# Performance work log

Measured on AMD Instinct MI355X. Metric: run time of the kernel, lower is better.

Reference implementation:

```python
import jax, jax.numpy as jnp
import numpy as np

D_MODEL = 1024
N_HEADS = 16
HEAD_DIM = 64  # 16*64 = 1024
LATENT = 256   # low-rank KV compression dim
NUM_WHEELS = 4
WHEEL_OUT = 256


def setup_inputs() -> dict:
    key = jax.random.key(0)
    ks = jax.random.split(key, 9)
    S = 2048
    s = lambda fan_in: 1.0 / np.sqrt(fan_in)
    return {
        "sketch_emb": jax.random.normal(ks[0], (S, D_MODEL), dtype=jnp.float32),
        "Wq": jax.random.normal(ks[1], (D_MODEL, N_HEADS * HEAD_DIM), dtype=jnp.float32) * s(D_MODEL),
        "Wdkv": jax.random.normal(ks[2], (D_MODEL, LATENT), dtype=jnp.float32) * s(D_MODEL),
        "Wuk": jax.random.normal(ks[3], (LATENT, N_HEADS * HEAD_DIM), dtype=jnp.float32) * s(LATENT),
        "Wuv": jax.random.normal(ks[4], (LATENT, N_HEADS * HEAD_DIM), dtype=jnp.float32) * s(LATENT),
        "Wo": jax.random.normal(ks[5], (N_HEADS * HEAD_DIM, D_MODEL), dtype=jnp.float32) * s(N_HEADS * HEAD_DIM),
        "wheel_W": jax.random.normal(ks[6], (NUM_WHEELS, D_MODEL, WHEEL_OUT), dtype=jnp.float32) * s(D_MODEL),
        "wheel_b": jax.random.normal(ks[7], (NUM_WHEELS, WHEEL_OUT), dtype=jnp.float32) * 0.01,
    }


def reference(sketch_emb, Wq, Wdkv, Wuk, Wuv, Wo, wheel_W, wheel_b):
    S = sketch_emb.shape[0]
    # Multi-head latent attention: per-head Q, shared low-rank KV latent.
    q = (sketch_emb @ Wq).reshape(S, N_HEADS, HEAD_DIM)          # [S,H,D]
    c_kv = sketch_emb @ Wdkv                                      # [S,L]
    k = (c_kv @ Wuk).reshape(S, N_HEADS, HEAD_DIM)                # [S,H,D]
    v = (c_kv @ Wuv).reshape(S, N_HEADS, HEAD_DIM)                # [S,H,D]
    scale = 1.0 / np.sqrt(HEAD_DIM).astype(np.float32)
    scores = jnp.einsum("qhd,khd->hqk", q, k) * scale             # [H,S,S]
    attn = jax.nn.softmax(scores, axis=-1)
    ctx = jnp.einsum("hqk,khd->qhd", attn, v).reshape(S, N_HEADS * HEAD_DIM)
    body = ctx @ Wo                                               # [S,1024]
    # Wheel projections batched as one einsum, then laid out as concat order
    # cat([body, w0, w1, w2, w3], dim=1)
    wheels = jnp.einsum("sd,wde->swe", body, wheel_W) + wheel_b   # [S,W,256]
    wheels = wheels.reshape(S, NUM_WHEELS * WHEEL_OUT)
    return jnp.concatenate([body, wheels], axis=1)                # [S,2048]
```

## Files before the change

### kernel.cpp

```cpp
#include <hip/hip_runtime.h>
#include <math.h>

#define S_LEN 2048
#define DMODEL 1024
#define NHEADS 16
#define HDIM 64
#define QPITCH 1280

typedef _Float16 f16x8 __attribute__((ext_vector_type(8)));
typedef _Float16 f16x4 __attribute__((ext_vector_type(4)));
typedef float    f32x4 __attribute__((ext_vector_type(4)));

__device__ __forceinline__ void gld_lds16(void* lds, const void* g) {
    __builtin_amdgcn_global_load_lds(
        (__attribute__((address_space(1))) void*)(g),
        (__attribute__((address_space(3))) void*)(lds), 16, 0, 0);
}

__device__ __forceinline__ void gemm_core(
    _Float16* sA, _Float16* sB,
    const _Float16* __restrict__ A, int lda,
    const _Float16* __restrict__ Bt, int ldb,
    int nkt,
    _Float16* __restrict__ Cb, int ldcb, int bmode,
    _Float16* __restrict__ Cb2, int ldcb2,
    int bx, int by)
{
    const int tid  = threadIdx.x;
    const int lane = tid & 63;
    const int w    = tid >> 6;
    const int quad = lane >> 4;
    const int c0   = lane & 15;
    const int m0 = by * 128;
    const int n0 = bx * 128;

    const int srow = lane >> 3;
    const int sc   = lane & 7;
    const _Float16* a_src[4]; const _Float16* b_src[4];
    int dstoff[4];
#pragma unroll
    for (int t = 0; t < 4; t++) {
        const int row = w * 32 + t * 8 + srow;
        const int c = sc ^ (row & 7);
        a_src[t] = A  + (size_t)(m0 + row) * lda + c * 8;
        b_src[t] = Bt + (size_t)(n0 + row) * ldb + c * 8;
        dstoff[t] = (w * 32 + t * 8) * 64;
    }

    const int mw = (w & 1) * 64;
    const int nw = (w >> 1) * 64;
    int arow[4], brow[4];
#pragma unroll
    for (int i = 0; i < 4; i++) {
        arow[i] = mw + i * 16 + c0;
        brow[i] = nw + i * 16 + c0;
    }

    f32x4 acc[4][4];
#pragma unroll
    for (int i = 0; i < 4; i++)
#pragma unroll
        for (int j = 0; j < 4; j++) acc[i][j] = (f32x4){0.f, 0.f, 0.f, 0.f};

    auto stage = [&](int buf) {
#pragma unroll
        for (int t = 0; t < 4; t++) {
            gld_lds16(&sA[buf * 8192 + dstoff[t]], a_src[t]); a_src[t] += 64;
            gld_lds16(&sB[buf * 8192 + dstoff[t]], b_src[t]); b_src[t] += 64;
        }
    };
    auto step = [&](int buf) {
#pragma unroll
        for (int ks = 0; ks < 2; ks++) {
            const int cb = ks * 4 + quad;
            f16x8 af[4], bfv[4];
#pragma unroll
            for (int i = 0; i < 4; i++)
                af[i] = *(const f16x8*)&sA[buf * 8192 + arow[i] * 64 + ((cb ^ (arow[i] & 7)) << 3)];
#pragma unroll
            for (int j = 0; j < 4; j++)
                bfv[j] = *(const f16x8*)&sB[buf * 8192 + brow[j] * 64 + ((cb ^ (brow[j] & 7)) << 3)];
#pragma unroll
            for (int i = 0; i < 4; i++)
#pragma unroll
                for (int j = 0; j < 4; j++)
                    acc[i][j] = __builtin_amdgcn_mfma_f32_16x16x32_f16(af[i], bfv[j], acc[i][j], 0, 0, 0);
        }
    };

    stage(0);
    for (int kt = 0; kt < nkt; kt += 2) {
        __syncthreads();
        stage(1);
        step(0);
        __syncthreads();
        if (kt + 2 < nkt) stage(0);
        step(1);
    }

#pragma unroll
    for (int i = 0; i < 4; i++) {
#pragma unroll
        for (int reg = 0; reg < 4; reg++) {
            const int m = m0 + mw + i * 16 + quad * 4 + reg;
#pragma unroll
            for (int j = 0; j < 4; j++) {
                const int n = n0 + nw + j * 16 + c0;
                _Float16 hv = (_Float16)acc[i][j][reg];
                if (bmode == 0) {
                    Cb[(size_t)m * ldcb + n] = hv;
                } else {
                    if (n < 1024) Cb[(size_t)m * ldcb + n] = hv;
                    else {
                        const int col = (m & ~63) | (((m & 15) << 2) | ((m >> 4) & 3));
                        Cb2[(size_t)(n - 1024) * ldcb2 + col] = hv;
                    }
                }
            }
        }
    }
}

__global__ __launch_bounds__(256) void gemm_qcwf(
    const _Float16* __restrict__ WcT, const _Float16* __restrict__ Wo_f16,
    _Float16* __restrict__ BtWheels,
    const _Float16* __restrict__ emb_f16, const _Float16* __restrict__ Wqc_t,
    _Float16* __restrict__ qc_f16)
{
    __shared__ _Float16 sA[2][8192];
    __shared__ _Float16 sB[2][8192];
    int b = blockIdx.x;
    if (b < 64) {
        gemm_core(&sA[0][0], &sB[0][0], WcT, 1024, Wo_f16, 1024, 16,
                  BtWheels, 1024, 0, nullptr, 0, b & 7, b >> 3);
    } else {
        b -= 64;
        gemm_core(&sA[0][0], &sB[0][0], emb_f16, 1024, Wqc_t, 1024, 16,
                  qc_f16, 1280, 0, nullptr, 0, b % 10, b / 10);
    }
}

__global__ __launch_bounds__(256) void gemm_kv(
    const _Float16* __restrict__ qc_f16, const _Float16* __restrict__ Wukv_t,
    _Float16* __restrict__ k_f16, _Float16* __restrict__ vT_f16)
{
    __shared__ _Float16 sA[2][8192];
    __shared__ _Float16 sB[2][8192];
    const int b = blockIdx.x;
    gemm_core(&sA[0][0], &sB[0][0], qc_f16 + 1024, 1280, Wukv_t, 256, 4,
              k_f16, 1024, 4, vT_f16, 2048, b & 15, b >> 4);
}

__global__ __launch_bounds__(256) void gemm_fin64(
    const _Float16* __restrict__ A,
    const _Float16* __restrict__ Bt,
    float* __restrict__ out,
    const float* __restrict__ bias)
{
    __shared__ _Float16 sA[2][64 * 64];
    __shared__ _Float16 sB[2][128 * 64];

    const int tid  = threadIdx.x;
    const int lane = tid & 63;
    const int w    = tid >> 6;
    const int quad = lane >> 4;
    const int c0   = lane & 15;
    const int m0 = blockIdx.y * 64;
    const int n0 = blockIdx.x * 128;

    const int srow = lane >> 3;
    const int sc   = lane & 7;
    const _Float16* a_src[2]; int a_dst[2];
#pragma unroll
    for (int t = 0; t < 2; t++) {
        const int row = t * 32 + w * 8 + srow;
        const int c = sc ^ (row & 7);
        a_src[t] = A + (size_t)(m0 + row) * 1024 + c * 8;
        a_dst[t] = (t * 32 + w * 8) * 64;
    }
    const _Float16* b_src[4]; int b_dst[4];
#pragma unroll
    for (int t = 0; t < 4; t++) {
        const int row = t * 32 + w * 8 + srow;
        const int c = sc ^ (row & 7);
        b_src[t] = Bt + (size_t)(n0 + row) * 1024 + c * 8;
        b_dst[t] = (t * 32 + w * 8) * 64;
    }

    const int mw = (w & 1) * 32;
    const int nw = (w >> 1) * 64;
    int arow[2], brow[4];
#pragma unroll
    for (int i = 0; i < 2; i++) arow[i] = mw + i * 16 + c0;
#pragma unroll
    for (int j = 0; j < 4; j++) brow[j] = nw + j * 16 + c0;

    f32x4 acc[2][4];
#pragma unroll
    for (int i = 0; i < 2; i++)
#pragma unroll
        for (int j = 0; j < 4; j++) acc[i][j] = (f32x4){0.f, 0.f, 0.f, 0.f};

    auto stage = [&](int buf) {
#pragma unroll
        for (int t = 0; t < 2; t++) { gld_lds16(&sA[buf][a_dst[t]], a_src[t]); a_src[t] += 64; }
#pragma unroll
        for (int t = 0; t < 4; t++) { gld_lds16(&sB[buf][b_dst[t]], b_src[t]); b_src[t] += 64; }
    };
    auto step = [&](int buf) {
#pragma unroll
        for (int ks = 0; ks < 2; ks++) {
            const int cb = ks * 4 + quad;
            f16x8 af[2], bfv[4];
#pragma unroll
            for (int i = 0; i < 2; i++)
                af[i] = *(const f16x8*)&sA[buf][arow[i] * 64 + ((cb ^ (arow[i] & 7)) << 3)];
#pragma unroll
            for (int j = 0; j < 4; j++)
                bfv[j] = *(const f16x8*)&sB[buf][brow[j] * 64 + ((cb ^ (brow[j] & 7)) << 3)];
#pragma unroll
            for (int i = 0; i < 2; i++)
#pragma unroll
                for (int j = 0; j < 4; j++)
                    acc[i][j] = __builtin_amdgcn_mfma_f32_16x16x32_f16(af[i], bfv[j], acc[i][j], 0, 0, 0);
        }
    };

    stage(0);
    for (int kt = 0; kt < 16; kt += 2) {
        __syncthreads();
        stage(1);
        step(0);
        __syncthreads();
        if (kt + 2 < 16) stage(0);
        step(1);
    }

    float bias_v[4];
#pragma unroll
    for (int j = 0; j < 4; j++) bias_v[j] = bias[n0 + nw + j * 16 + c0];
#pragma unroll
    for (int i = 0; i < 2; i++) {
#pragma unroll
        for (int reg = 0; reg < 4; reg++) {
            const int m = m0 + mw + i * 16 + quad * 4 + reg;
#pragma unroll
            for (int j = 0; j < 4; j++) {
                const int n = n0 + nw + j * 16 + c0;
                out[(size_t)m * 2048 + n] = acc[i][j][reg] + bias_v[j];
            }
        }
    }
}

#define PITCH 72
#define SOFT_M0 6.0f

__global__ __launch_bounds__(256) void attn_mfma_kernel(
    const _Float16* __restrict__ qs,
    const _Float16* __restrict__ kk,
    const _Float16* __restrict__ vT,
    float* __restrict__ Opart,
    float* __restrict__ lpart)
{
    __shared__ _Float16 Ks[2][64 * 64];
    __shared__ _Float16 Vt[2][64 * 64];
    __shared__ _Float16 Ps[4 * 32 * PITCH];

    const int qb = blockIdx.x;
    const int h  = blockIdx.y;
    const int kz = blockIdx.z;
    const int tid  = threadIdx.x;
    const int lane = tid & 63;
    const int w    = tid >> 6;
    const int quad = lane >> 4;
    const int c0   = lane & 15;

    f16x8 qfrag[2][2];
#pragma unroll
    for (int m = 0; m < 2; m++) {
        const _Float16* qrow = qs + (size_t)(qb * 128 + w * 32 + m * 16 + c0) * QPITCH + h * HDIM;
        qfrag[m][0] = *(const f16x8*)(qrow + quad * 8);
        qfrag[m][1] = *(const f16x8*)(qrow + 32 + quad * 8);
    }

    const int srow = lane >> 3;
    const int sc   = lane & 7;
    const _Float16* k_src[2]; const _Float16* v_src[2];
    int dstoff[2];
#pragma unroll
    for (int t = 0; t < 2; t++) {
        const int row = w * 16 + t * 8 + srow;
        const int c = sc ^ (row & 7);
        k_src[t] = kk + (size_t)(kz * 1024 + row) * DMODEL + h * HDIM + c * 8;
        v_src[t] = vT + (size_t)(h * HDIM + row) * S_LEN + kz * 1024 + c * 8;
        dstoff[t] = (w * 16 + t * 8) * 64;
    }

    f32x4 Ofrag[2][4];
#pragma unroll
    for (int m = 0; m < 2; m++)
#pragma unroll
        for (int nb = 0; nb < 4; nb++) Ofrag[m][nb] = (f32x4){0.f, 0.f, 0.f, 0.f};
    float l_r[2][4] = {{0.f, 0.f, 0.f, 0.f}, {0.f, 0.f, 0.f, 0.f}};

    _Float16* Pw = Ps + w * (32 * PITCH);

    auto stage = [&](int buf) {
#pragma unroll
        for (int t = 0; t < 2; t++) {
            gld_lds16(&Ks[buf][dstoff[t]], k_src[t]); k_src[t] += (size_t)64 * DMODEL;
            gld_lds16(&Vt[buf][dstoff[t]], v_src[t]); v_src[t] += 64;
        }
    };

    auto attn_step = [&](int buf) {
        f32x4 sfrag[2][4];
#pragma unroll
        for (int m = 0; m < 2; m++)
#pragma unroll
            for (int nb = 0; nb < 4; nb++) sfrag[m][nb] = (f32x4){0.f, 0.f, 0.f, 0.f};
#pragma unroll
        for (int nb = 0; nb < 4; nb++) {
            const int n = nb * 16 + c0;
#pragma unroll
            for (int ks = 0; ks < 2; ks++) {
                const int cb = ks * 4 + quad;
                f16x8 kfr = *(const f16x8*)&Ks[buf][n * 64 + ((cb ^ (n & 7)) << 3)];
#pragma unroll
                for (int m = 0; m < 2; m++)
                    sfrag[m][nb] = __builtin_amdgcn_mfma_f32_16x16x32_f16(qfrag[m][ks], kfr, sfrag[m][nb], 0, 0, 0);
            }
        }

#pragma unroll
        for (int m = 0; m < 2; m++)
#pragma unroll
            for (int reg = 0; reg < 4; reg++) {
                float p0 = __expf(sfrag[m][0][reg] - SOFT_M0);
                float p1 = __expf(sfrag[m][1][reg] - SOFT_M0);
                float p2 = __expf(sfrag[m][2][reg] - SOFT_M0);
                float p3 = __expf(sfrag[m][3][reg] - SOFT_M0);
                sfrag[m][0][reg] = p0; sfrag[m][1][reg] = p1;
                sfrag[m][2][reg] = p2; sfrag[m][3][reg] = p3;
                l_r[m][reg] += p0 + p1 + p2 + p3;
            }

#pragma unroll
        for (int m = 0; m < 2; m++)
#pragma unroll
            for (int reg = 0; reg < 4; reg++) {
                const int prow = m * 16 + quad * 4 + reg;
                f16x4 pv;
                pv[0] = (_Float16)sfrag[m][0][reg];
                pv[1] = (_Float16)sfrag[m][1][reg];
                pv[2] = (_Float16)sfrag[m][2][reg];
                pv[3] = (_Float16)sfrag[m][3][reg];
                *(f16x4*)&Pw[prow * PITCH + c0 * 4] = pv;
            }
        __asm__ __volatile__("s_waitcnt lgkmcnt(0)" ::: "memory");

        f16x8 pfrag[2][2];
#pragma unroll
        for (int m = 0; m < 2; m++)
#pragma unroll
            for (int ks = 0; ks < 2; ks++)
                pfrag[m][ks] = *(const f16x8*)&Pw[(m * 16 + c0) * PITCH + ks * 32 + quad * 8];

#pragma unroll
        for (int nb = 0; nb < 4; nb++) {
            const int n = nb * 16 + c0;
#pragma unroll
            for (int ks = 0; ks < 2; ks++) {
                const int cb = ks * 4 + quad;
                f16x8 vf = *(const f16x8*)&Vt[buf][n * 64 + ((cb ^ (n & 7)) << 3)];
#pragma unroll
                for (int m = 0; m < 2; m++)
                    Ofrag[m][nb] = __builtin_amdgcn_mfma_f32_16x16x32_f16(pfrag[m][ks], vf, Ofrag[m][nb], 0, 0, 0);
            }
        }
    };

    stage(0);
    for (int kt = 0; kt < 16; kt += 2) {
        __syncthreads();
        stage(1);
        attn_step(0);
        __syncthreads();
        if (kt + 2 < 16) stage(0);
        attn_step(1);
    }

#pragma unroll
    for (int m = 0; m < 2; m++) {
#pragma unroll
        for (int reg = 0; reg < 4; reg++) {
            const int row = qb * 128 + w * 32 + m * 16 + quad * 4 + reg;
            float rsum = l_r[m][reg];
#pragma unroll
            for (int mask = 1; mask < 16; mask <<= 1)
                rsum += __shfl_xor(rsum, mask, 64);
            if (c0 == 0) lpart[(size_t)(kz * 16 + h) * 2048 + row] = rsum;
            float* op = Opart + ((size_t)kz * 2048 + row) * 1024 + h * HDIM;
#pragma unroll
            for (int nb = 0; nb < 4; nb++)
                op[nb * 16 + c0] = Ofrag[m][nb][reg];
        }
    }
}

__global__ __launch_bounds__(256) void attn_combine_kernel(
    const float* __restrict__ Opart, const float* __restrict__ lpart,
    _Float16* __restrict__ ctx)
{
    const int i = blockIdx.x * 256 + threadIdx.x;
    const int row = i >> 8;
    const int c4  = (i & 255) * 4;
    const int h = c4 >> 6;
    const float l = lpart[(size_t)h * 2048 + row] + lpart[(size_t)(16 + h) * 2048 + row];
    const float inv = 1.0f / l;
    float4 o0 = ((const float4*)(Opart + (size_t)row * 1024))[c4 >> 2];
    float4 o1 = ((const float4*)(Opart + (size_t)(2048 + row) * 1024))[c4 >> 2];
    f16x4 v;
    v[0] = (_Float16)((o0.x + o1.x) * inv);
    v[1] = (_Float16)((o0.y + o1.y) * inv);
    v[2] = (_Float16)((o0.z + o1.z) * inv);
    v[3] = (_Float16)((o0.w + o1.w) * inv);
    *(f16x4*)(ctx + (size_t)row * 1024 + c4) = v;
}

__device__ __forceinline__ void xpose_seg(float (*tile)[33],
    const float* __restrict__ src, _Float16* __restrict__ dst,
    int C, int dpitch, float scale, int bx, int by, int nbase0)
{
    const int r0 = by * 32, c0 = bx * 32;
    const int tr = threadIdx.x >> 5, tc = threadIdx.x & 31;
#pragma unroll
    for (int i = 0; i < 4; i++)
        tile[tr + i * 8][tc] = src[(size_t)(r0 + tr + i * 8) * C + c0 + tc];
    __syncthreads();
    const int nr = threadIdx.x & 31;
    const int k0 = (threadIdx.x >> 5) * 4;
    f16x4 hv;
#pragma unroll
    for (int e = 0; e < 4; e++)
        hv[e] = (_Float16)(tile[k0 + e][nr] * scale);
    *(f16x4*)(dst + (size_t)(nbase0 + c0 + nr) * dpitch + (r0 + k0)) = hv;
}

__global__ __launch_bounds__(256) void megaprep_kernel(
    const float* __restrict__ emb, const float* __restrict__ Wq,
    const float* __restrict__ Wdkv, const float* __restrict__ Wuk,
    const float* __restrict__ Wuv, const float* __restrict__ Wo,
    const float* __restrict__ wheelW, const float* __restrict__ wheelB,
    _Float16* __restrict__ Wqc_t, _Float16* __restrict__ Wukv_t,
    _Float16* __restrict__ Bt_full, _Float16* __restrict__ WcT,
    _Float16* __restrict__ Wo_f16, _Float16* __restrict__ emb_f16,
    float* __restrict__ biasbuf)
{
    __shared__ float tile[32][33];
    int b = blockIdx.x;
    const int tid = threadIdx.x;

    if (b < 1024) { xpose_seg(tile, Wq, Wqc_t, 1024, 1024, 0.125f, b & 31, b >> 5, 0); return; }
    b -= 1024;
    if (b < 256)  { xpose_seg(tile, Wdkv, Wqc_t + 1048576, 256, 1024, 1.f, b & 7, b >> 3, 0); return; }
    b -= 256;
    if (b < 256)  { xpose_seg(tile, Wuk, Wukv_t, 1024, 256, 1.f, b & 31, b >> 5, 0); return; }
    b -= 256;
    if (b < 256)  { xpose_seg(tile, Wuv, Wukv_t + 262144, 1024, 256, 1.f, b & 31, b >> 5, 0); return; }
    b -= 256;
    if (b < 1024) { xpose_seg(tile, Wo, Bt_full, 1024, 1024, 1.f, b & 31, b >> 5, 0); return; }
    b -= 1024;
    if (b < 1024) {
        const int z = b >> 8, rem = b & 255;
        xpose_seg(tile, wheelW + (size_t)z * 262144, WcT, 256, 1024, 1.f,
                  rem & 7, rem >> 3, z * 256);
        return;
    }
    b -= 1024;
    if (b < 1024) {
        const int i = b * 256 + tid;
        float4 f = ((const float4*)Wo)[i];
        f16x4 v;
        v[0] = (_Float16)f.x; v[1] = (_Float16)f.y;
        v[2] = (_Float16)f.z; v[3] = (_Float16)f.w;
        ((f16x4*)Wo_f16)[i] = v;
        return;
    }
    b -= 1024;
    if (b < 2048) {
        const int i = b * 256 + tid;
        float4 f = ((const float4*)emb)[i];
        f16x4 v;
        v[0] = (_Float16)f.x; v[1] = (_Float16)f.y;
        v[2] = (_Float16)f.z; v[3] = (_Float16)f.w;
        ((f16x4*)emb_f16)[i] = v;
        return;
    }
    b -= 2048;
    if (b < 8) {
        const int i = b * 256 + tid;
        biasbuf[i] = (i < 1024) ? 0.f : wheelB[i - 1024];
    }
}

extern "C" void kernel_launch(void* const* d_in, const int* in_sizes, int n_in,
                              void* d_out, int out_size, void* d_ws, size_t ws_size,
                              hipStream_t stream) {
    const float* emb    = (const float*)d_in[0];
    const float* Wq     = (const float*)d_in[1];
    const float* Wdkv   = (const float*)d_in[2];
    const float* Wuk    = (const float*)d_in[3];
    const float* Wuv    = (const float*)d_in[4];
    const float* Wo     = (const float*)d_in[5];
    const float* wheelW = (const float*)d_in[6];
    const float* wheelB = (const float*)d_in[7];
    float* out = (float*)d_out;

    _Float16* ws = (_Float16*)d_ws;
    _Float16* Bt_full = ws;
    _Float16* Wqc_t   = ws + 2097152;
    _Float16* Wukv_t  = ws + 3407872;
    float*    biasbuf = (float*)(ws + 3932160);
    _Float16* WcT     = ws + 3936256;
    _Float16* Wo_f16  = ws + 4984832;
    _Float16* ctx     = ws + 3936256;
    _Float16* emb_f16 = ws + 6033408;
    _Float16* qc_f16  = ws + 8130560;
    _Float16* k_f16   = ws + 10752000;
    _Float16* vT_f16  = ws + 12849152;
    float*    Opart   = (float*)(ws + 14946304);
    float*    lpart   = (float*)(ws + 23334912);

    megaprep_kernel<<<6920, 256, 0, stream>>>(
        emb, Wq, Wdkv, Wuk, Wuv, Wo, wheelW, wheelB,
        Wqc_t, Wukv_t, Bt_full, WcT, Wo_f16, emb_f16, biasbuf);

    gemm_qcwf<<<224, 256, 0, stream>>>(WcT, Wo_f16, Bt_full + (size_t)1024 * 1024,
                                       emb_f16, Wqc_t, qc_f16);

    gemm_kv<<<256, 256, 0, stream>>>(qc_f16, Wukv_t, k_f16, vT_f16);

    attn_mfma_kernel<<<dim3(16, 16, 2), 256, 0, stream>>>(qc_f16, k_f16, vT_f16, Opart, lpart);

    attn_combine_kernel<<<2048, 256, 0, stream>>>(Opart, lpart, ctx);

    gemm_fin64<<<dim3(16, 32), 256, 0, stream>>>(ctx, Bt_full, out, biasbuf);
}
```

Before: 175.0 us.

## Remap block indices for XCD locality, use exp2 softmax, add MFMA priority hints

Block-to-tile mappings in the GEMM kernels and the attention kernel are remapped: grids are flattened and swizzled so blocks sharing operands land on the same XCD, aiming for better L2 reuse. The softmax switches from __expf to the native exp2 instruction, with log2(e) folded into the Wuk weights during prep and a matching constant offset. s_setprio hints are placed around the MFMA loops. The changes are independent, and the new index mappings rely on fixed grid sizes.

```diff
diff --git a/kernel.cpp b/kernel.cpp
--- a/kernel.cpp
+++ b/kernel.cpp
@@ -132,11 +132,11 @@
     int b = blockIdx.x;
     if (b < 64) {
         gemm_core(&sA[0][0], &sB[0][0], WcT, 1024, Wo_f16, 1024, 16,
-                  BtWheels, 1024, 0, nullptr, 0, b & 7, b >> 3);
+                  BtWheels, 1024, 0, nullptr, 0, b >> 3, b & 7);
     } else {
         b -= 64;
         gemm_core(&sA[0][0], &sB[0][0], emb_f16, 1024, Wqc_t, 1024, 16,
-                  qc_f16, 1280, 0, nullptr, 0, b % 10, b / 10);
+                  qc_f16, 1280, 0, nullptr, 0, b >> 4, b & 15);
     }
 }
 
@@ -148,7 +148,7 @@
     __shared__ _Float16 sB[2][8192];
     const int b = blockIdx.x;
     gemm_core(&sA[0][0], &sB[0][0], qc_f16 + 1024, 1280, Wukv_t, 256, 4,
-              k_f16, 1024, 4, vT_f16, 2048, b & 15, b >> 4);
+              k_f16, 1024, 4, vT_f16, 2048, b >> 4, b & 15);
 }
 
 __global__ __launch_bounds__(256) void gemm_fin64(
@@ -165,8 +165,14 @@
     const int w    = tid >> 6;
     const int quad = lane >> 4;
     const int c0   = lane & 15;
-    const int m0 = blockIdx.y * 64;
-    const int n0 = blockIdx.x * 128;
+
+    const int flat = blockIdx.x;
+    const int xcd  = flat & 7;
+    const int wi   = flat >> 3;
+    const int by   = (xcd & 3) * 8 + (wi & 7);
+    const int bx   = (xcd >> 2) * 8 + (wi >> 3);
+    const int m0 = by * 64;
+    const int n0 = bx * 128;
 
     const int srow = lane >> 3;
     const int sc   = lane & 7;
@@ -254,7 +260,7 @@
 }
 
 #define PITCH 72
-#define SOFT_M0 6.0f
+#define SOFT_M2 8.65617024533378f
 
 __global__ __launch_bounds__(256) void attn_mfma_kernel(
     const _Float16* __restrict__ qs,
@@ -267,9 +273,11 @@
     __shared__ _Float16 Vt[2][64 * 64];
     __shared__ _Float16 Ps[4 * 32 * PITCH];
 
-    const int qb = blockIdx.x;
-    const int h  = blockIdx.y;
-    const int kz = blockIdx.z;
+    const int flat = blockIdx.x;
+    const int g  = flat & 31;
+    const int qb = flat >> 5;
+    const int h  = g & 15;
+    const int kz = g >> 4;
     const int tid  = threadIdx.x;
     const int lane = tid & 63;
     const int w    = tid >> 6;
@@ -320,6 +328,7 @@
         for (int m = 0; m < 2; m++)
 #pragma unroll
             for (int nb = 0; nb < 4; nb++) sfrag[m][nb] = (f32x4){0.f, 0.f, 0.f, 0.f};
+        __builtin_amdgcn_s_setprio(1);
 #pragma unroll
         for (int nb = 0; nb < 4; nb++) {
             const int n = nb * 16 + c0;
@@ -332,15 +341,16 @@
                     sfrag[m][nb] = __builtin_amdgcn_mfma_f32_16x16x32_f16(qfrag[m][ks], kfr, sfrag[m][nb], 0, 0, 0);
             }
         }
+        __builtin_amdgcn_s_setprio(0);
 
 #pragma unroll
         for (int m = 0; m < 2; m++)
 #pragma unroll
             for (int reg = 0; reg < 4; reg++) {
-                float p0 = __expf(sfrag[m][0][reg] - SOFT_M0);
-                float p1 = __expf(sfrag[m][1][reg] - SOFT_M0);
-                float p2 = __expf(sfrag[m][2][reg] - SOFT_M0);
-                float p3 = __expf(sfrag[m][3][reg] - SOFT_M0);
+                float p0 = __builtin_amdgcn_exp2f(sfrag[m][0][reg] - SOFT_M2);
+                float p1 = __builtin_amdgcn_exp2f(sfrag[m][1][reg] - SOFT_M2);
+                float p2 = __builtin_amdgcn_exp2f(sfrag[m][2][reg] - SOFT_M2);
+                float p3 = __builtin_amdgcn_exp2f(sfrag[m][3][reg] - SOFT_M2);
                 sfrag[m][0][reg] = p0; sfrag[m][1][reg] = p1;
                 sfrag[m][2][reg] = p2; sfrag[m][3][reg] = p3;
                 l_r[m][reg] += p0 + p1 + p2 + p3;
@@ -367,6 +377,7 @@
             for (int ks = 0; ks < 2; ks++)
                 pfrag[m][ks] = *(const f16x8*)&Pw[(m * 16 + c0) * PITCH + ks * 32 + quad * 8];
 
+        __builtin_amdgcn_s_setprio(1);
 #pragma unroll
         for (int nb = 0; nb < 4; nb++) {
             const int n = nb * 16 + c0;
@@ -379,6 +390,7 @@
                     Ofrag[m][nb] = __builtin_amdgcn_mfma_f32_16x16x32_f16(pfrag[m][ks], vf, Ofrag[m][nb], 0, 0, 0);
             }
         }
+        __builtin_amdgcn_s_setprio(0);
     };
 
     stage(0);
@@ -466,7 +478,7 @@
     b -= 1024;
     if (b < 256)  { xpose_seg(tile, Wdkv, Wqc_t + 1048576, 256, 1024, 1.f, b & 7, b >> 3, 0); return; }
     b -= 256;
-    if (b < 256)  { xpose_seg(tile, Wuk, Wukv_t, 1024, 256, 1.f, b & 31, b >> 5, 0); return; }
+    if (b < 256)  { xpose_seg(tile, Wuk, Wukv_t, 1024, 256, 1.4426950408889634f, b & 31, b >> 5, 0); return; }
     b -= 256;
     if (b < 256)  { xpose_seg(tile, Wuv, Wukv_t + 262144, 1024, 256, 1.f, b & 31, b >> 5, 0); return; }
     b -= 256;
@@ -542,9 +554,9 @@
 
     gemm_kv<<<256, 256, 0, stream>>>(qc_f16, Wukv_t, k_f16, vT_f16);
 
-    attn_mfma_kernel<<<dim3(16, 16, 2), 256, 0, stream>>>(qc_f16, k_f16, vT_f16, Opart, lpart);
+    attn_mfma_kernel<<<512, 256, 0, stream>>>(qc_f16, k_f16, vT_f16, Opart, lpart);
 
     attn_combine_kernel<<<2048, 256, 0, stream>>>(Opart, lpart, ctx);
 
-    gemm_fin64<<<dim3(16, 32), 256, 0, stream>>>(ctx, Bt_full, out, biasbuf);
-}
+    gemm_fin64<<<512, 256, 0, stream>>>(ctx, Bt_full, out, biasbuf);
+}
```

New measurement: 171.4 us. 1.02x faster.
